# Optimization experiments

Measured on AMD Instinct MI355X. Metric: run time of the kernel, lower is better.

Reference implementation:

```python
import jax, jax.numpy as jnp
import numpy as np

N_CLASSES = 16
N_CATEGORY = 4096
OUT = 512
BS = 4096


def setup_inputs() -> dict:
    key = jax.random.key(0)
    k1, k2, k3 = jax.random.split(key, 3)
    batch = jax.random.normal(k1, (BS, N_CATEGORY), dtype=jnp.float32)
    classes = jax.random.randint(k2, (BS,), 0, N_CLASSES, dtype=jnp.int32)
    # Stacked per-class Linear weights, each [out, in] like nn.Linear.weight.
    W = jax.random.normal(k3, (N_CLASSES, OUT, N_CATEGORY), dtype=jnp.float32) * 0.02
    return {"batch": batch, "classes": classes, "W": W}


def reference(batch, classes, W):
    # Original: result[i] = W[classes[i]] @ batch[i]  (per-sample class-indexed linear).
    # Vectorized: compute all experts' outputs [b, c, o], then select per-sample class.
    all_out = jnp.einsum('bi,coi->bco', batch, W)
    out = jnp.take_along_axis(all_out, classes.astype(jnp.int32)[:, None, None], axis=1)
    return out[:, 0, :]  # [bs, out]
```

## Files before the change

kernel.cpp:

```cpp
#include <hip/hip_runtime.h>
#include <hip/hip_bf16.h>

typedef __attribute__((ext_vector_type(4))) float f32x4;
typedef __attribute__((ext_vector_type(8))) short s16x8;

#define NCLS 16
#define NCAT 4096
#define NOUT 512
#define NBS  4096

#define BM 128
#define BN 128
#define BK 64
#define NSPLIT 2
#define KSPLIT (NCAT / NSPLIT)
#define MAXTILES 48

#define WS_NT    0
#define WS_CBASE 1
#define WS_TCLS  32
#define WS_TM0   96
#define WS_SIDX  160

__global__ __launch_bounds__(256) void prep_kernel(const int* __restrict__ cls,
                                                   int* __restrict__ ws) {
  __shared__ int cnt[NCLS];
  __shared__ int cur[NCLS];
  __shared__ int cb[NCLS + 1];
  const int t = threadIdx.x;
  if (t < NCLS) { cnt[t] = 0; cur[t] = 0; }
  __syncthreads();
  for (int i = t; i < NBS; i += 256) atomicAdd(&cnt[cls[i]], 1);
  __syncthreads();
  if (t == 0) {
    int acc = 0, nt = 0;
    for (int c = 0; c < NCLS; ++c) {
      cb[c] = acc;
      ws[WS_CBASE + c] = acc;
      for (int m0 = 0; m0 < cnt[c]; m0 += BM) {
        ws[WS_TCLS + nt] = c;
        ws[WS_TM0 + nt] = m0;
        ++nt;
      }
      acc += cnt[c];
    }
    cb[NCLS] = acc;
    ws[WS_CBASE + NCLS] = acc;
    ws[WS_NT] = nt;
  }
  __syncthreads();
  for (int i = t; i < NBS; i += 256) {
    int c = cls[i];
    int p = atomicAdd(&cur[c], 1);
    ws[WS_SIDX + cb[c] + p] = i;
  }
}

__device__ __forceinline__ void pk2(float x0, float x1, unsigned& hb, unsigned& lb) {
  __hip_bfloat162 h2 = __float22bfloat162_rn(make_float2(x0, x1));
  float2 hf = __bfloat1622float2(h2);
  __hip_bfloat162 l2 = __float22bfloat162_rn(make_float2(x0 - hf.x, x1 - hf.y));
  __builtin_memcpy(&hb, &h2, 4);
  __builtin_memcpy(&lb, &l2, 4);
}

__device__ __forceinline__ void cvt8(float4 a, float4 b, uint4& hi, uint4& lo) {
  pk2(a.x, a.y, hi.x, lo.x);
  pk2(a.z, a.w, hi.y, lo.y);
  pk2(b.x, b.y, hi.z, lo.z);
  pk2(b.z, b.w, hi.w, lo.w);
}

__global__ __launch_bounds__(256) void gemm_kernel(const float* __restrict__ batch,
                                                   const float* __restrict__ W,
                                                   const int* __restrict__ ws,
                                                   float* __restrict__ out) {
  const int tile = blockIdx.x;
  if (tile >= ws[WS_NT]) return;
  const int c    = ws[WS_TCLS + tile];
  const int m0   = ws[WS_TM0 + tile];
  const int base = ws[WS_CBASE + c];
  const int Mc   = ws[WS_CBASE + c + 1] - base;
  const int n0   = blockIdx.y * BN;
  const int k0   = blockIdx.z * KSPLIT;
  const int* sidx = ws + WS_SIDX + base;

  __shared__ char lds[4 * BM * BK * 2];
  char* const Ahi = lds;
  char* const Alo = lds + 16384;
  char* const Bhi = lds + 32768;
  char* const Blo = lds + 49152;

  const int t = threadIdx.x;
  const int r = t >> 1;
  const int h = t & 1;
  const int arow = sidx[min(m0 + r, Mc - 1)];
  const float* aptr = batch + (size_t)arow * NCAT + k0 + h * 32;
  const float* bptr = W + ((size_t)c * NOUT + (n0 + r)) * NCAT + k0 + h * 32;
  const int wswz = (r & 4) << 3;

  const int lane = t & 63;
  const int wv   = t >> 6;
  const int wm   = (wv >> 1) * 64;
  const int wn   = (wv & 1) * 64;
  const int l15  = lane & 15;
  const int kg16 = (lane >> 4) * 16;

  f32x4 acc[4][4];
  #pragma unroll
  for (int i = 0; i < 4; ++i)
    #pragma unroll
    for (int j = 0; j < 4; ++j) acc[i][j] = (f32x4){0.f, 0.f, 0.f, 0.f};

  for (int kt = 0; kt < KSPLIT; kt += BK) {
    __syncthreads();
    #pragma unroll
    for (int cc = 0; cc < 4; ++cc) {
      const int koff = kt + cc * 8;
      float4 a0 = *(const float4*)(aptr + koff);
      float4 a1 = *(const float4*)(aptr + koff + 4);
      float4 b0 = *(const float4*)(bptr + koff);
      float4 b1 = *(const float4*)(bptr + koff + 4);
      uint4 ah, al, bh, bl;
      cvt8(a0, a1, ah, al);
      cvt8(b0, b1, bh, bl);
      const int off = r * 128 + ((h * 64 + cc * 16) ^ wswz);
      *(uint4*)(Ahi + off) = ah;
      *(uint4*)(Alo + off) = al;
      *(uint4*)(Bhi + off) = bh;
      *(uint4*)(Blo + off) = bl;
    }
    __syncthreads();
    #pragma unroll
    for (int ks = 0; ks < 2; ++ks) {
      s16x8 ahf[4], alf[4], bhf[4], blf[4];
      #pragma unroll
      for (int i = 0; i < 4; ++i) {
        const int m = wm + i * 16 + l15;
        const int offa = m * 128 + ((ks * 64 + kg16) ^ ((m & 4) << 3));
        ahf[i] = *(const s16x8*)(Ahi + offa);
        alf[i] = *(const s16x8*)(Alo + offa);
        const int n = wn + i * 16 + l15;
        const int offb = n * 128 + ((ks * 64 + kg16) ^ ((n & 4) << 3));
        bhf[i] = *(const s16x8*)(Bhi + offb);
        blf[i] = *(const s16x8*)(Blo + offb);
      }
      #pragma unroll
      for (int i = 0; i < 4; ++i)
        #pragma unroll
        for (int j = 0; j < 4; ++j) {
          acc[i][j] = __builtin_amdgcn_mfma_f32_16x16x32_bf16(ahf[i], bhf[j], acc[i][j], 0, 0, 0);
          acc[i][j] = __builtin_amdgcn_mfma_f32_16x16x32_bf16(ahf[i], blf[j], acc[i][j], 0, 0, 0);
          acc[i][j] = __builtin_amdgcn_mfma_f32_16x16x32_bf16(alf[i], bhf[j], acc[i][j], 0, 0, 0);
        }
    }
  }

  const int r4 = (lane >> 4) * 4;
  #pragma unroll
  for (int i = 0; i < 4; ++i) {
    #pragma unroll
    for (int jj = 0; jj < 4; ++jj) {
      const int mloc = wm + i * 16 + r4 + jj;
      const int gm = m0 + mloc;
      if (gm < Mc) {
        const int sample = sidx[gm];
        float* orow = out + (size_t)sample * NOUT + n0 + wn;
        #pragma unroll
        for (int j = 0; j < 4; ++j) {
          atomicAdd(orow + j * 16 + l15, acc[i][j][jj]);
        }
      }
    }
  }
}

extern "C" void kernel_launch(void* const* d_in, const int* in_sizes, int n_in,
                              void* d_out, int out_size, void* d_ws, size_t ws_size,
                              hipStream_t stream) {
  const float* batch = (const float*)d_in[0];
  const int*   cls   = (const int*)d_in[1];
  const float* W     = (const float*)d_in[2];
  float* out = (float*)d_out;
  int*   ws  = (int*)d_ws;

  prep_kernel<<<1, 256, 0, stream>>>(cls, ws);
  hipMemsetAsync(d_out, 0, (size_t)out_size * sizeof(float), stream);
  gemm_kernel<<<dim3(MAXTILES, NOUT / BN, NSPLIT), 256, 0, stream>>>(batch, W, ws, out);
}
```

Baseline: 369.8 us.

## Prefetch next K tile into registers, widen split-K, improve LDS swizzle and prep

The GEMM main loop now loads the next BK chunk of A and B from global memory into registers while the current chunk is being converted and consumed, so load latency overlaps with MFMA work. Split-K rises from 2 to 4 to launch more blocks, and launch bounds request 2 blocks per CU. The LDS XOR swizzle now uses 3 row bits instead of 1 to cut bank conflicts. The prep kernel replaces shared atomics with per-thread counting and a prefix scan. In exchange, prefetch registers raise register pressure, and the larger split doubles the atomic output adds.

Measured after the change: 365.8 us. Within noise of the previous version (-1.1%).

```diff
diff --git a/kernel.cpp b/kernel.cpp
--- a/kernel.cpp
+++ b/kernel.cpp
@@ -12,8 +12,9 @@
 #define BM 128
 #define BN 128
 #define BK 64
-#define NSPLIT 2
+#define NSPLIT 4
 #define KSPLIT (NCAT / NSPLIT)
+#define NITER  (KSPLIT / BK)
 #define MAXTILES 48
 
 #define WS_NT    0
@@ -24,35 +25,62 @@
 
 __global__ __launch_bounds__(256) void prep_kernel(const int* __restrict__ cls,
                                                    int* __restrict__ ws) {
-  __shared__ int cnt[NCLS];
-  __shared__ int cur[NCLS];
-  __shared__ int cb[NCLS + 1];
+  __shared__ int lcnt[NCLS * 256];
+  __shared__ int cb[NCLS];
+  __shared__ int ctot[NCLS];
   const int t = threadIdx.x;
-  if (t < NCLS) { cnt[t] = 0; cur[t] = 0; }
+
+  int cl[16];
+  #pragma unroll
+  for (int j = 0; j < 16; ++j) cl[j] = cls[j * 256 + t];
+
+  int cnt[NCLS];
+  #pragma unroll
+  for (int c = 0; c < NCLS; ++c) cnt[c] = 0;
+  #pragma unroll
+  for (int j = 0; j < 16; ++j) {
+    #pragma unroll
+    for (int c = 0; c < NCLS; ++c) cnt[c] += (cl[j] == c) ? 1 : 0;
+  }
+  #pragma unroll
+  for (int c = 0; c < NCLS; ++c) lcnt[c * 256 + t] = cnt[c];
   __syncthreads();
-  for (int i = t; i < NBS; i += 256) atomicAdd(&cnt[cls[i]], 1);
+
+  if (t < NCLS) {
+    int run = 0;
+    for (int u = 0; u < 256; ++u) {
+      int v = lcnt[t * 256 + u];
+      lcnt[t * 256 + u] = run;
+      run += v;
+    }
+    ctot[t] = run;
+  }
   __syncthreads();
+
   if (t == 0) {
-    int acc = 0, nt = 0;
+    int acc = 0, nt_ = 0;
     for (int c = 0; c < NCLS; ++c) {
       cb[c] = acc;
       ws[WS_CBASE + c] = acc;
-      for (int m0 = 0; m0 < cnt[c]; m0 += BM) {
-        ws[WS_TCLS + nt] = c;
-        ws[WS_TM0 + nt] = m0;
-        ++nt;
-      }
-      acc += cnt[c];
-    }
-    cb[NCLS] = acc;
+      for (int m0 = 0; m0 < ctot[c]; m0 += BM) {
+        ws[WS_TCLS + nt_] = c;
+        ws[WS_TM0 + nt_] = m0;
+        ++nt_;
+      }
+      acc += ctot[c];
+    }
     ws[WS_CBASE + NCLS] = acc;
-    ws[WS_NT] = nt;
+    ws[WS_NT] = nt_;
   }
   __syncthreads();
-  for (int i = t; i < NBS; i += 256) {
-    int c = cls[i];
-    int p = atomicAdd(&cur[c], 1);
-    ws[WS_SIDX + cb[c] + p] = i;
+
+  #pragma unroll
+  for (int j = 0; j < 16; ++j) {
+    int c = cl[j];
+    int within = 0;
+    #pragma unroll
+    for (int j2 = 0; j2 < 16; ++j2) within += (j2 < j && cl[j2] == c) ? 1 : 0;
+    ws[WS_SIDX + cb[c] + lcnt[c * 256 + t] + within] = j * 256 + t;
   }
 }
 
@@ -71,10 +99,10 @@
   pk2(b.z, b.w, hi.w, lo.w);
 }
 
-__global__ __launch_bounds__(256) void gemm_kernel(const float* __restrict__ batch,
-                                                   const float* __restrict__ W,
-                                                   const int* __restrict__ ws,
-                                                   float* __restrict__ out) {
+__global__ __launch_bounds__(256, 2) void gemm_kernel(const float* __restrict__ batch,
+                                                      const float* __restrict__ W,
+                                                      const int* __restrict__ ws,
+                                                      float* __restrict__ out) {
   const int tile = blockIdx.x;
   if (tile >= ws[WS_NT]) return;
   const int c    = ws[WS_TCLS + tile];
@@ -97,7 +125,7 @@
   const int arow = sidx[min(m0 + r, Mc - 1)];
   const float* aptr = batch + (size_t)arow * NCAT + k0 + h * 32;
   const float* bptr = W + ((size_t)c * NOUT + (n0 + r)) * NCAT + k0 + h * 32;
-  const int wswz = (r & 4) << 3;
+  const int wswz = (r & 7) << 4;
 
   const int lane = t & 63;
   const int wv   = t >> 6;
@@ -112,24 +140,40 @@
     #pragma unroll
     for (int j = 0; j < 4; ++j) acc[i][j] = (f32x4){0.f, 0.f, 0.f, 0.f};
 
-  for (int kt = 0; kt < KSPLIT; kt += BK) {
+  float4 pa0[4], pa1[4], pb0[4], pb1[4];
+  #pragma unroll
+  for (int cc = 0; cc < 4; ++cc) {
+    const int ko = cc * 8;
+    pa0[cc] = *(const float4*)(aptr + ko);
+    pa1[cc] = *(const float4*)(aptr + ko + 4);
+    pb0[cc] = *(const float4*)(bptr + ko);
+    pb1[cc] = *(const float4*)(bptr + ko + 4);
+  }
+
+  for (int it = 0; it < NITER; ++it) {
     __syncthreads();
     #pragma unroll
     for (int cc = 0; cc < 4; ++cc) {
-      const int koff = kt + cc * 8;
-      float4 a0 = *(const float4*)(aptr + koff);
-      float4 a1 = *(const float4*)(aptr + koff + 4);
-      float4 b0 = *(const float4*)(bptr + koff);
-      float4 b1 = *(const float4*)(bptr + koff + 4);
       uint4 ah, al, bh, bl;
-      cvt8(a0, a1, ah, al);
-      cvt8(b0, b1, bh, bl);
+      cvt8(pa0[cc], pa1[cc], ah, al);
+      cvt8(pb0[cc], pb1[cc], bh, bl);
       const int off = r * 128 + ((h * 64 + cc * 16) ^ wswz);
       *(uint4*)(Ahi + off) = ah;
       *(uint4*)(Alo + off) = al;
       *(uint4*)(Bhi + off) = bh;
       *(uint4*)(Blo + off) = bl;
     }
+    if (it + 1 < NITER) {
+      const int kt = (it + 1) * BK;
+      #pragma unroll
+      for (int cc = 0; cc < 4; ++cc) {
+        const int ko = kt + cc * 8;
+        pa0[cc] = *(const float4*)(aptr + ko);
+        pa1[cc] = *(const float4*)(aptr + ko + 4);
+        pb0[cc] = *(const float4*)(bptr + ko);
+        pb1[cc] = *(const float4*)(bptr + ko + 4);
+      }
+    }
     __syncthreads();
     #pragma unroll
     for (int ks = 0; ks < 2; ++ks) {
@@ -137,11 +181,11 @@
       #pragma unroll
       for (int i = 0; i < 4; ++i) {
         const int m = wm + i * 16 + l15;
-        const int offa = m * 128 + ((ks * 64 + kg16) ^ ((m & 4) << 3));
+        const int offa = m * 128 + ((ks * 64 + kg16) ^ ((m & 7) << 4));
         ahf[i] = *(const s16x8*)(Ahi + offa);
         alf[i] = *(const s16x8*)(Alo + offa);
         const int n = wn + i * 16 + l15;
-        const int offb = n * 128 + ((ks * 64 + kg16) ^ ((n & 4) << 3));
+        const int offb = n * 128 + ((ks * 64 + kg16) ^ ((n & 7) << 4));
         bhf[i] = *(const s16x8*)(Bhi + offb);
         blf[i] = *(const s16x8*)(Blo + offb);
       }
```
